# Kernel optimization log

Measured on AMD Instinct MI355X. Metric: run time of the kernel, lower is better.

## Reference

```python
import jax, jax.numpy as jnp
import numpy as np

B, T = 4096, 16384

def setup_inputs() -> dict:
    key = jax.random.key(0)
    ks = jax.random.split(key, 6)
    x = jax.random.normal(ks[0], (B, T), dtype=jnp.float32)
    v0 = jnp.zeros((B, 2), dtype=jnp.float32)
    # match torch init ranges: b* ~ U(-1,1), a* ~ U(-0.5,0.5) (stable region)
    b0 = jax.random.uniform(ks[1], (1,), jnp.float32, -1.0, 1.0)
    b1 = jax.random.uniform(ks[2], (1,), jnp.float32, -1.0, 1.0)
    b2 = jax.random.uniform(ks[3], (1,), jnp.float32, -1.0, 1.0)
    a1 = jax.random.uniform(ks[4], (1,), jnp.float32, -0.5, 0.5)
    a2 = jax.random.uniform(ks[5], (1,), jnp.float32, -0.5, 0.5)
    return {"x": x, "v0": v0, "b0": b0, "b1": b1, "b2": b2, "a1": a1, "a2": a2}

def reference(x, v0, b0, b1, b2, a1, a2):
    """DF-II transposed biquad, scanned over time.
    x: [B, T] input samples; v0: [B, 2] initial state.
    Returns (y [B, T], v_final [B, 2]).
    Per-step math is exactly DTDFIICell.forward:
      y   = x_t * b0 + v[:,0]
      v0' = x_t * b1 + v[:,1] - y * a1
      v1' = x_t * b2            - y * a2
    """
    def step(v, xt):  # v: [B,2], xt: [B]
        y = xt * b0 + v[:, 0]                      # [B]
        v_new = jnp.stack(
            [xt * b1 + v[:, 1] - y * a1,
             xt * b2 - y * a2], axis=-1)           # [B,2]
        return v_new, y
    v_final, ys = jax.lax.scan(step, v0, x.T)      # ys: [T, B]
    return ys.T, v_final
```

## Files before the change

kernel.cpp:

```cpp
#include <hip/hip_runtime.h>

#define B_DIM 4096
#define T_DIM 16384
#define WAVES_PER_BLOCK 4
#define PER_LANE 8
#define CHUNK (64 * PER_LANE)
#define NIT (T_DIM / CHUNK)
#define VSTEP (CHUNK / 4)

typedef float f32x4 __attribute__((ext_vector_type(4)));

struct M2 { float a, b, c, d; };

__device__ inline M2 m2mul(const M2& X, const M2& Y) {
    M2 r;
    r.a = fmaf(X.a, Y.a, X.b * Y.c);
    r.b = fmaf(X.a, Y.b, X.b * Y.d);
    r.c = fmaf(X.c, Y.a, X.d * Y.c);
    r.d = fmaf(X.c, Y.b, X.d * Y.d);
    return r;
}

__global__ __launch_bounds__(256) void biquad_scan_kernel(
    const float* __restrict__ x, const float* __restrict__ v0in,
    const float* __restrict__ pb0, const float* __restrict__ pb1,
    const float* __restrict__ pb2, const float* __restrict__ pa1,
    const float* __restrict__ pa2,
    float* __restrict__ y, float* __restrict__ vout)
{
    const int lane = threadIdx.x & 63;
    const int wave = threadIdx.x >> 6;
    const int row  = blockIdx.x * WAVES_PER_BLOCK + wave;
    if (row >= B_DIM) return;

    const float b0 = *pb0, b1 = *pb1, b2 = *pb2, a1 = *pa1, a2 = *pa2;
    const float na1 = -a1, na2 = -a2;
    const float c0 = b1 - a1 * b0;
    const float c1 = b2 - a2 * b0;

    M2 A  { na1, 1.0f, na2, 0.0f };
    M2 A2 = m2mul(A, A);
    M2 A4 = m2mul(A2, A2);
    M2 A8 = m2mul(A4, A4);

    M2 S0, S1, S2, S3, S4, S5;
    M2 Q { 1.f, 0.f, 0.f, 1.f };
    M2 M = A8;
    S0 = M; if (lane & 1)  Q = m2mul(M, Q); M = m2mul(M, M);
    S1 = M; if (lane & 2)  Q = m2mul(M, Q); M = m2mul(M, M);
    S2 = M; if (lane & 4)  Q = m2mul(M, Q); M = m2mul(M, M);
    S3 = M; if (lane & 8)  Q = m2mul(M, Q); M = m2mul(M, M);
    S4 = M; if (lane & 16) Q = m2mul(M, Q); M = m2mul(M, M);
    S5 = M; if (lane & 32) Q = m2mul(M, Q); M = m2mul(M, M);
    const M2 R = M;

    const float* xr = x + (size_t)row * T_DIM;
    float*       yr = y + (size_t)row * T_DIM;

    float vc0 = v0in[row * 2 + 0];
    float vc1 = v0in[row * 2 + 1];

    const f32x4* xp = (const f32x4*)xr + 2 * lane;
    f32x4*       yp = (f32x4*)yr + 2 * lane;

    f32x4 xa  = xp[0],     xb  = xp[1];
    f32x4 nxa = xp[VSTEP], nxb = xp[VSTEP + 1];

    for (int i = 0; i < NIT; ++i) {
        f32x4 mxa = {0.f, 0.f, 0.f, 0.f}, mxb = {0.f, 0.f, 0.f, 0.f};
        if (i + 2 < NIT) {
            mxa = xp[(size_t)(i + 2) * VSTEP];
            mxb = xp[(size_t)(i + 2) * VSTEP + 1];
        }

        float d0 = c0 * xa[0];
        float d1 = c1 * xa[0];
        #define FOLD(xs)                                               \
        {   float t0 = fmaf(c0, (xs), fmaf(na1, d0, d1));              \
            float t1 = fmaf(na2, d0, c1 * (xs));                       \
            d0 = t0; d1 = t1; }
        FOLD(xa[1]) FOLD(xa[2]) FOLD(xa[3])
        FOLD(xb[0]) FOLD(xb[1]) FOLD(xb[2]) FOLD(xb[3])
        #undef FOLD

        #define SCAN_STEP(Sm, o)                                        \
        {   float q0 = __shfl_up(d0, (unsigned)(o));                    \
            float q1 = __shfl_up(d1, (unsigned)(o));                    \
            if (lane < (o)) { q0 = 0.f; q1 = 0.f; }                     \
            float t0 = fmaf(Sm.a, q0, fmaf(Sm.b, q1, d0));              \
            float t1 = fmaf(Sm.c, q0, fmaf(Sm.d, q1, d1));              \
            d0 = t0; d1 = t1; }
        SCAN_STEP(S0, 1)
        SCAN_STEP(S1, 2)
        SCAN_STEP(S2, 4)
        SCAN_STEP(S3, 8)
        SCAN_STEP(S4, 16)
        SCAN_STEP(S5, 32)
        #undef SCAN_STEP

        float e0 = __shfl_up(d0, 1u);
        float e1 = __shfl_up(d1, 1u);
        if (lane == 0) { e0 = 0.f; e1 = 0.f; }

        float v0r = fmaf(Q.a, vc0, fmaf(Q.b, vc1, e0));
        float v1r = fmaf(Q.c, vc0, fmaf(Q.d, vc1, e1));

        f32x4 yo0, yo1;
        #define REPLAY(xs, dst)                                        \
        {   float yy = fmaf((xs), b0, v0r);                            \
            float n0 = fmaf(na1, yy, fmaf((xs), b1, v1r));             \
            float n1 = fmaf(na2, yy, (xs) * b2);                       \
            v0r = n0; v1r = n1; dst = yy; }
        REPLAY(xa[0], yo0[0]) REPLAY(xa[1], yo0[1])
        REPLAY(xa[2], yo0[2]) REPLAY(xa[3], yo0[3])
        REPLAY(xb[0], yo1[0]) REPLAY(xb[1], yo1[1])
        REPLAY(xb[2], yo1[2]) REPLAY(xb[3], yo1[3])
        #undef REPLAY

        yp[(size_t)i * VSTEP]     = yo0;
        yp[(size_t)i * VSTEP + 1] = yo1;

        float t0 = __shfl(d0, 63);
        float t1 = __shfl(d1, 63);
        float nv0 = fmaf(R.a, vc0, fmaf(R.b, vc1, t0));
        float nv1 = fmaf(R.c, vc0, fmaf(R.d, vc1, t1));
        vc0 = nv0; vc1 = nv1;

        xa = nxa; xb = nxb; nxa = mxa; nxb = mxb;
    }

    if (lane == 0) {
        vout[row * 2 + 0] = vc0;
        vout[row * 2 + 1] = vc1;
    }
}

extern "C" void kernel_launch(void* const* d_in, const int* in_sizes, int n_in,
                              void* d_out, int out_size, void* d_ws, size_t ws_size,
                              hipStream_t stream) {
    const float* x   = (const float*)d_in[0];
    const float* v0  = (const float*)d_in[1];
    const float* b0  = (const float*)d_in[2];
    const float* b1  = (const float*)d_in[3];
    const float* b2  = (const float*)d_in[4];
    const float* a1  = (const float*)d_in[5];
    const float* a2  = (const float*)d_in[6];

    float* y    = (float*)d_out;
    float* vout = (float*)d_out + (size_t)B_DIM * T_DIM;

    dim3 grid(B_DIM / WAVES_PER_BLOCK);
    dim3 block(64 * WAVES_PER_BLOCK);
    biquad_scan_kernel<<<grid, block, 0, stream>>>(x, v0, b0, b1, b2, a1, a2, y, vout);
}
```

Baseline: 118.5 us.

## Split each chunk into two independent 256-sample scans with coalesced float4 access

Each iteration's 512-sample chunk is now two 256-sample halves, with each lane taking 4 contiguous samples per half instead of 8. Lanes therefore read and write consecutive float4s, which makes the global accesses fully coalesced. The two halves are folded, scanned and replayed as independent chains, so their instructions can interleave and hide latency. The cost is twice as many shuffles per chunk and an extra serial state hop between the halves, with the lookback powers recomputed starting from A^4.

After: 118.0 us. No clear change (-0.4%).

```diff
diff --git a/kernel.cpp b/kernel.cpp
--- a/kernel.cpp
+++ b/kernel.cpp
@@ -3,8 +3,7 @@
 #define B_DIM 4096
 #define T_DIM 16384
 #define WAVES_PER_BLOCK 4
-#define PER_LANE 8
-#define CHUNK (64 * PER_LANE)
+#define CHUNK 512
 #define NIT (T_DIM / CHUNK)
 #define VSTEP (CHUNK / 4)
 
@@ -41,11 +40,10 @@
     M2 A  { na1, 1.0f, na2, 0.0f };
     M2 A2 = m2mul(A, A);
     M2 A4 = m2mul(A2, A2);
-    M2 A8 = m2mul(A4, A4);
 
     M2 S0, S1, S2, S3, S4, S5;
     M2 Q { 1.f, 0.f, 0.f, 1.f };
-    M2 M = A8;
+    M2 M = A4;
     S0 = M; if (lane & 1)  Q = m2mul(M, Q); M = m2mul(M, M);
     S1 = M; if (lane & 2)  Q = m2mul(M, Q); M = m2mul(M, M);
     S2 = M; if (lane & 4)  Q = m2mul(M, Q); M = m2mul(M, M);
@@ -60,73 +58,85 @@
     float vc0 = v0in[row * 2 + 0];
     float vc1 = v0in[row * 2 + 1];
 
-    const f32x4* xp = (const f32x4*)xr + 2 * lane;
-    f32x4*       yp = (f32x4*)yr + 2 * lane;
+    const f32x4* xp = (const f32x4*)xr;
+    f32x4*       yp = (f32x4*)yr;
 
-    f32x4 xa  = xp[0],     xb  = xp[1];
-    f32x4 nxa = xp[VSTEP], nxb = xp[VSTEP + 1];
+    f32x4 cA = xp[lane],         cB = xp[64 + lane];
+    f32x4 nA = xp[VSTEP + lane], nB = xp[VSTEP + 64 + lane];
 
     for (int i = 0; i < NIT; ++i) {
-        f32x4 mxa = {0.f, 0.f, 0.f, 0.f}, mxb = {0.f, 0.f, 0.f, 0.f};
+        f32x4 mA = {0.f, 0.f, 0.f, 0.f}, mB = {0.f, 0.f, 0.f, 0.f};
         if (i + 2 < NIT) {
-            mxa = xp[(size_t)(i + 2) * VSTEP];
-            mxb = xp[(size_t)(i + 2) * VSTEP + 1];
+            mA = xp[(size_t)(i + 2) * VSTEP + lane];
+            mB = xp[(size_t)(i + 2) * VSTEP + 64 + lane];
         }
 
-        float d0 = c0 * xa[0];
-        float d1 = c1 * xa[0];
-        #define FOLD(xs)                                               \
-        {   float t0 = fmaf(c0, (xs), fmaf(na1, d0, d1));              \
-            float t1 = fmaf(na2, d0, c1 * (xs));                       \
-            d0 = t0; d1 = t1; }
-        FOLD(xa[1]) FOLD(xa[2]) FOLD(xa[3])
-        FOLD(xb[0]) FOLD(xb[1]) FOLD(xb[2]) FOLD(xb[3])
-        #undef FOLD
+        float dA0 = c0 * cA[0], dA1 = c1 * cA[0];
+        float dB0 = c0 * cB[0], dB1 = c1 * cB[0];
+        #define FOLD2(xsA, xsB)                                          \
+        {   float tA0 = fmaf(c0, (xsA), fmaf(na1, dA0, dA1));            \
+            float tA1 = fmaf(na2, dA0, c1 * (xsA));                      \
+            float tB0 = fmaf(c0, (xsB), fmaf(na1, dB0, dB1));            \
+            float tB1 = fmaf(na2, dB0, c1 * (xsB));                      \
+            dA0 = tA0; dA1 = tA1; dB0 = tB0; dB1 = tB1; }
+        FOLD2(cA[1], cB[1]) FOLD2(cA[2], cB[2]) FOLD2(cA[3], cB[3])
+        #undef FOLD2
 
-        #define SCAN_STEP(Sm, o)                                        \
-        {   float q0 = __shfl_up(d0, (unsigned)(o));                    \
-            float q1 = __shfl_up(d1, (unsigned)(o));                    \
-            if (lane < (o)) { q0 = 0.f; q1 = 0.f; }                     \
-            float t0 = fmaf(Sm.a, q0, fmaf(Sm.b, q1, d0));              \
-            float t1 = fmaf(Sm.c, q0, fmaf(Sm.d, q1, d1));              \
-            d0 = t0; d1 = t1; }
-        SCAN_STEP(S0, 1)
-        SCAN_STEP(S1, 2)
-        SCAN_STEP(S2, 4)
-        SCAN_STEP(S3, 8)
-        SCAN_STEP(S4, 16)
-        SCAN_STEP(S5, 32)
-        #undef SCAN_STEP
+        #define SCAN2(Sm, o)                                             \
+        {   float qA0 = __shfl_up(dA0, (unsigned)(o));                   \
+            float qA1 = __shfl_up(dA1, (unsigned)(o));                   \
+            float qB0 = __shfl_up(dB0, (unsigned)(o));                   \
+            float qB1 = __shfl_up(dB1, (unsigned)(o));                   \
+            if (lane < (o)) { qA0 = 0.f; qA1 = 0.f; qB0 = 0.f; qB1 = 0.f; } \
+            float tA0 = fmaf(Sm.a, qA0, fmaf(Sm.b, qA1, dA0));           \
+            float tA1 = fmaf(Sm.c, qA0, fmaf(Sm.d, qA1, dA1));           \
+            float tB0 = fmaf(Sm.a, qB0, fmaf(Sm.b, qB1, dB0));           \
+            float tB1 = fmaf(Sm.c, qB0, fmaf(Sm.d, qB1, dB1));           \
+            dA0 = tA0; dA1 = tA1; dB0 = tB0; dB1 = tB1; }
+        SCAN2(S0, 1)
+        SCAN2(S1, 2)
+        SCAN2(S2, 4)
+        SCAN2(S3, 8)
+        SCAN2(S4, 16)
+        SCAN2(S5, 32)
+        #undef SCAN2
 
-        float e0 = __shfl_up(d0, 1u);
-        float e1 = __shfl_up(d1, 1u);
-        if (lane == 0) { e0 = 0.f; e1 = 0.f; }
+        float eA0 = __shfl_up(dA0, 1u), eA1 = __shfl_up(dA1, 1u);
+        float eB0 = __shfl_up(dB0, 1u), eB1 = __shfl_up(dB1, 1u);
+        if (lane == 0) { eA0 = 0.f; eA1 = 0.f; eB0 = 0.f; eB1 = 0.f; }
 
-        float v0r = fmaf(Q.a, vc0, fmaf(Q.b, vc1, e0));
-        float v1r = fmaf(Q.c, vc0, fmaf(Q.d, vc1, e1));
+        const float TA0 = __shfl(dA0, 63), TA1 = __shfl(dA1, 63);
+        const float TB0 = __shfl(dB0, 63), TB1 = __shfl(dB1, 63);
 
-        f32x4 yo0, yo1;
-        #define REPLAY(xs, dst)                                        \
-        {   float yy = fmaf((xs), b0, v0r);                            \
-            float n0 = fmaf(na1, yy, fmaf((xs), b1, v1r));             \
-            float n1 = fmaf(na2, yy, (xs) * b2);                       \
-            v0r = n0; v1r = n1; dst = yy; }
-        REPLAY(xa[0], yo0[0]) REPLAY(xa[1], yo0[1])
-        REPLAY(xa[2], yo0[2]) REPLAY(xa[3], yo0[3])
-        REPLAY(xb[0], yo1[0]) REPLAY(xb[1], yo1[1])
-        REPLAY(xb[2], yo1[2]) REPLAY(xb[3], yo1[3])
-        #undef REPLAY
+        float vA0 = fmaf(Q.a, vc0, fmaf(Q.b, vc1, eA0));
+        float vA1 = fmaf(Q.c, vc0, fmaf(Q.d, vc1, eA1));
+        const float sB0 = fmaf(R.a, vc0, fmaf(R.b, vc1, TA0));
+        const float sB1 = fmaf(R.c, vc0, fmaf(R.d, vc1, TA1));
+        float vB0 = fmaf(Q.a, sB0, fmaf(Q.b, sB1, eB0));
+        float vB1 = fmaf(Q.c, sB0, fmaf(Q.d, sB1, eB1));
 
-        yp[(size_t)i * VSTEP]     = yo0;
-        yp[(size_t)i * VSTEP + 1] = yo1;
+        f32x4 yoA, yoB;
+        #define REPLAY2(k)                                               \
+        {   float xsA = cA[k], xsB = cB[k];                              \
+            float yyA = fmaf(xsA, b0, vA0);                              \
+            float yyB = fmaf(xsB, b0, vB0);                              \
+            float nA0 = fmaf(na1, yyA, fmaf(xsA, b1, vA1));              \
+            float nA1 = fmaf(na2, yyA, xsA * b2);                        \
+            float nB0 = fmaf(na1, yyB, fmaf(xsB, b1, vB1));              \
+            float nB1 = fmaf(na2, yyB, xsB * b2);                        \
+            vA0 = nA0; vA1 = nA1; vB0 = nB0; vB1 = nB1;                  \
+            yoA[k] = yyA; yoB[k] = yyB; }
+        REPLAY2(0) REPLAY2(1) REPLAY2(2) REPLAY2(3)
+        #undef REPLAY2
 
-        float t0 = __shfl(d0, 63);
-        float t1 = __shfl(d1, 63);
-        float nv0 = fmaf(R.a, vc0, fmaf(R.b, vc1, t0));
-        float nv1 = fmaf(R.c, vc0, fmaf(R.d, vc1, t1));
+        yp[(size_t)i * VSTEP + lane]      = yoA;
+        yp[(size_t)i * VSTEP + 64 + lane] = yoB;
+
+        const float nv0 = fmaf(R.a, sB0, fmaf(R.b, sB1, TB0));
+        const float nv1 = fmaf(R.c, sB0, fmaf(R.d, sB1, TB1));
         vc0 = nv0; vc1 = nv1;
 
-        xa = nxa; xb = nxb; nxa = mxa; nxb = mxb;
+        cA = nA; cB = nB; nA = mA; nB = mB;
     }
 
     if (lane == 0) {
```

## Use DPP row shifts and broadcasts for the wave scan with 4 samples per lane

Applied to the files above, without the earlier changes.

Shrinks the per-lane chunk from 8 to 4 samples, giving 256-sample chunks and twice as many iterations. The cross-lane linear-recurrence scan switches from ds_bpermute-based __shfl_up to DPP row_shr steps within each row of 16 lanes, then row_bcast15/31 steps with precomputed transition matrices (P, G) to combine rows. The chunk total is read with readlane instead of a shuffle. This cuts shuffle latency on the serial chain per chunk but doubles the number of chunk iterations and uses 16-byte loads and stores per lane instead of 32-byte ones.

After: 114.5 us. 3.4% less time.

```diff
diff --git a/kernel.cpp b/kernel.cpp
--- a/kernel.cpp
+++ b/kernel.cpp
@@ -3,10 +3,8 @@
 #define B_DIM 4096
 #define T_DIM 16384
 #define WAVES_PER_BLOCK 4
-#define PER_LANE 8
-#define CHUNK (64 * PER_LANE)
+#define CHUNK 256
 #define NIT (T_DIM / CHUNK)
-#define VSTEP (CHUNK / 4)
 
 typedef float f32x4 __attribute__((ext_vector_type(4)));
 
@@ -20,6 +18,17 @@
     r.d = fmaf(X.c, Y.b, X.d * Y.d);
     return r;
 }
+
+template<int CTRL, int RMASK>
+__device__ inline float dpp0(float v) {
+    int r = __builtin_amdgcn_update_dpp(0, __builtin_bit_cast(int, v),
+                                        CTRL, RMASK, 0xf, true);
+    return __builtin_bit_cast(float, r);
+}
+
+#define DPP_ROW_SHR(N) (0x110 + (N))
+#define DPP_BCAST15    0x142
+#define DPP_BCAST31    0x143
 
 __global__ __launch_bounds__(256) void biquad_scan_kernel(
     const float* __restrict__ x, const float* __restrict__ v0in,
@@ -41,18 +50,32 @@
     M2 A  { na1, 1.0f, na2, 0.0f };
     M2 A2 = m2mul(A, A);
     M2 A4 = m2mul(A2, A2);
-    M2 A8 = m2mul(A4, A4);
 
     M2 S0, S1, S2, S3, S4, S5;
+    M2 M = A4;
+    S0 = M; M = m2mul(M, M);
+    S1 = M; M = m2mul(M, M);
+    S2 = M; M = m2mul(M, M);
+    S3 = M; M = m2mul(M, M);
+    S4 = M; M = m2mul(M, M);
+    S5 = M; M = m2mul(M, M);
+    const M2 R = M;
+
     M2 Q { 1.f, 0.f, 0.f, 1.f };
-    M2 M = A8;
-    S0 = M; if (lane & 1)  Q = m2mul(M, Q); M = m2mul(M, M);
-    S1 = M; if (lane & 2)  Q = m2mul(M, Q); M = m2mul(M, M);
-    S2 = M; if (lane & 4)  Q = m2mul(M, Q); M = m2mul(M, M);
-    S3 = M; if (lane & 8)  Q = m2mul(M, Q); M = m2mul(M, M);
-    S4 = M; if (lane & 16) Q = m2mul(M, Q); M = m2mul(M, M);
-    S5 = M; if (lane & 32) Q = m2mul(M, Q); M = m2mul(M, M);
-    const M2 R = M;
+    if (lane & 1)  Q = m2mul(S0, Q);
+    if (lane & 2)  Q = m2mul(S1, Q);
+    if (lane & 4)  Q = m2mul(S2, Q);
+    if (lane & 8)  Q = m2mul(S3, Q);
+    if (lane & 16) Q = m2mul(S4, Q);
+    if (lane & 32) Q = m2mul(S5, Q);
+
+    const int l4 = lane & 15;
+    M2 P = A4;
+    if (l4 & 1) P = m2mul(S0, P);
+    if (l4 & 2) P = m2mul(S1, P);
+    if (l4 & 4) P = m2mul(S2, P);
+    if (l4 & 8) P = m2mul(S3, P);
+    M2 G = (lane >= 48) ? m2mul(S4, P) : P;
 
     const float* xr = x + (size_t)row * T_DIM;
     float*       yr = y + (size_t)row * T_DIM;
@@ -60,43 +83,52 @@
     float vc0 = v0in[row * 2 + 0];
     float vc1 = v0in[row * 2 + 1];
 
-    const f32x4* xp = (const f32x4*)xr + 2 * lane;
-    f32x4*       yp = (f32x4*)yr + 2 * lane;
+    const f32x4* xp = (const f32x4*)xr;
+    f32x4*       yp = (f32x4*)yr;
 
-    f32x4 xa  = xp[0],     xb  = xp[1];
-    f32x4 nxa = xp[VSTEP], nxb = xp[VSTEP + 1];
+    f32x4 xv = xp[lane];
+    f32x4 xn = xp[64 + lane];
 
     for (int i = 0; i < NIT; ++i) {
-        f32x4 mxa = {0.f, 0.f, 0.f, 0.f}, mxb = {0.f, 0.f, 0.f, 0.f};
-        if (i + 2 < NIT) {
-            mxa = xp[(size_t)(i + 2) * VSTEP];
-            mxb = xp[(size_t)(i + 2) * VSTEP + 1];
-        }
+        f32x4 xm = {0.f, 0.f, 0.f, 0.f};
+        if (i + 2 < NIT) xm = xp[(size_t)(i + 2) * 64 + lane];
 
-        float d0 = c0 * xa[0];
-        float d1 = c1 * xa[0];
+        float d0 = c0 * xv[0];
+        float d1 = c1 * xv[0];
         #define FOLD(xs)                                               \
         {   float t0 = fmaf(c0, (xs), fmaf(na1, d0, d1));              \
             float t1 = fmaf(na2, d0, c1 * (xs));                       \
             d0 = t0; d1 = t1; }
-        FOLD(xa[1]) FOLD(xa[2]) FOLD(xa[3])
-        FOLD(xb[0]) FOLD(xb[1]) FOLD(xb[2]) FOLD(xb[3])
+        FOLD(xv[1]) FOLD(xv[2]) FOLD(xv[3])
         #undef FOLD
 
-        #define SCAN_STEP(Sm, o)                                        \
-        {   float q0 = __shfl_up(d0, (unsigned)(o));                    \
-            float q1 = __shfl_up(d1, (unsigned)(o));                    \
-            if (lane < (o)) { q0 = 0.f; q1 = 0.f; }                     \
-            float t0 = fmaf(Sm.a, q0, fmaf(Sm.b, q1, d0));              \
-            float t1 = fmaf(Sm.c, q0, fmaf(Sm.d, q1, d1));              \
+        #define SCAN_DPP(Sm, o)                                        \
+        {   float q0 = dpp0<DPP_ROW_SHR(o), 0xf>(d0);                  \
+            float q1 = dpp0<DPP_ROW_SHR(o), 0xf>(d1);                  \
+            float t0 = fmaf(Sm.a, q0, fmaf(Sm.b, q1, d0));             \
+            float t1 = fmaf(Sm.c, q0, fmaf(Sm.d, q1, d1));             \
             d0 = t0; d1 = t1; }
-        SCAN_STEP(S0, 1)
-        SCAN_STEP(S1, 2)
-        SCAN_STEP(S2, 4)
-        SCAN_STEP(S3, 8)
-        SCAN_STEP(S4, 16)
-        SCAN_STEP(S5, 32)
-        #undef SCAN_STEP
+        SCAN_DPP(S0, 1)
+        SCAN_DPP(S1, 2)
+        SCAN_DPP(S2, 4)
+        SCAN_DPP(S3, 8)
+        #undef SCAN_DPP
+
+        {   float q0 = dpp0<DPP_BCAST15, 0xa>(d0);
+            float q1 = dpp0<DPP_BCAST15, 0xa>(d1);
+            float t0 = fmaf(P.a, q0, fmaf(P.b, q1, d0));
+            float t1 = fmaf(P.c, q0, fmaf(P.d, q1, d1));
+            d0 = t0; d1 = t1; }
+        {   float q0 = dpp0<DPP_BCAST31, 0xc>(d0);
+            float q1 = dpp0<DPP_BCAST31, 0xc>(d1);
+            float t0 = fmaf(G.a, q0, fmaf(G.b, q1, d0));
+            float t1 = fmaf(G.c, q0, fmaf(G.d, q1, d1));
+            d0 = t0; d1 = t1; }
+
+        const float T0 = __builtin_bit_cast(float,
+            __builtin_amdgcn_readlane(__builtin_bit_cast(int, d0), 63));
+        const float T1 = __builtin_bit_cast(float,
+            __builtin_amdgcn_readlane(__builtin_bit_cast(int, d1), 63));
 
         float e0 = __shfl_up(d0, 1u);
         float e1 = __shfl_up(d1, 1u);
@@ -105,28 +137,23 @@
         float v0r = fmaf(Q.a, vc0, fmaf(Q.b, vc1, e0));
         float v1r = fmaf(Q.c, vc0, fmaf(Q.d, vc1, e1));
 
-        f32x4 yo0, yo1;
+        f32x4 yv;
         #define REPLAY(xs, dst)                                        \
         {   float yy = fmaf((xs), b0, v0r);                            \
             float n0 = fmaf(na1, yy, fmaf((xs), b1, v1r));             \
             float n1 = fmaf(na2, yy, (xs) * b2);                       \
             v0r = n0; v1r = n1; dst = yy; }
-        REPLAY(xa[0], yo0[0]) REPLAY(xa[1], yo0[1])
-        REPLAY(xa[2], yo0[2]) REPLAY(xa[3], yo0[3])
-        REPLAY(xb[0], yo1[0]) REPLAY(xb[1], yo1[1])
-        REPLAY(xb[2], yo1[2]) REPLAY(xb[3], yo1[3])
+        REPLAY(xv[0], yv[0]) REPLAY(xv[1], yv[1])
+        REPLAY(xv[2], yv[2]) REPLAY(xv[3], yv[3])
         #undef REPLAY
 
-        yp[(size_t)i * VSTEP]     = yo0;
-        yp[(size_t)i * VSTEP + 1] = yo1;
+        yp[(size_t)i * 64 + lane] = yv;
 
-        float t0 = __shfl(d0, 63);
-        float t1 = __shfl(d1, 63);
-        float nv0 = fmaf(R.a, vc0, fmaf(R.b, vc1, t0));
-        float nv1 = fmaf(R.c, vc0, fmaf(R.d, vc1, t1));
+        float nv0 = fmaf(R.a, vc0, fmaf(R.b, vc1, T0));
+        float nv1 = fmaf(R.c, vc0, fmaf(R.d, vc1, T1));
         vc0 = nv0; vc1 = nv1;
 
-        xa = nxa; xb = nxb; nxa = mxa; nxb = mxb;
+        xv = xn; xn = xm;
     }
 
     if (lane == 0) {
```

## Split each row across four waves with cross-wave carry via shared memory

Applied to the files above, without the earlier changes.

Each block now handles one row instead of four. The four waves each process consecutive 256-sample chunks of a 1024-sample super-chunk, with 4 samples per lane instead of 8. Wave carries are exchanged through double-buffered shared memory with a __syncthreads per super-chunk, and each wave composes the preceding waves' carries using the chunk transition matrix. This shortens each wave's serial fold and replay chain and increases row-level parallelism, but it adds a block barrier and LDS traffic every iteration, plus redundant carry composition.

After: 111.3 us. 1.06x faster.

```diff
diff --git a/kernel.cpp b/kernel.cpp
--- a/kernel.cpp
+++ b/kernel.cpp
@@ -2,11 +2,9 @@
 
 #define B_DIM 4096
 #define T_DIM 16384
-#define WAVES_PER_BLOCK 4
-#define PER_LANE 8
-#define CHUNK (64 * PER_LANE)
-#define NIT (T_DIM / CHUNK)
-#define VSTEP (CHUNK / 4)
+#define NWAVES 4
+#define CHUNK 256
+#define NSUP (T_DIM / (CHUNK * NWAVES))
 
 typedef float f32x4 __attribute__((ext_vector_type(4)));
 
@@ -29,9 +27,8 @@
     float* __restrict__ y, float* __restrict__ vout)
 {
     const int lane = threadIdx.x & 63;
-    const int wave = threadIdx.x >> 6;
-    const int row  = blockIdx.x * WAVES_PER_BLOCK + wave;
-    if (row >= B_DIM) return;
+    const int w    = threadIdx.x >> 6;
+    const int row  = blockIdx.x;
 
     const float b0 = *pb0, b1 = *pb1, b2 = *pb2, a1 = *pa1, a2 = *pa2;
     const float na1 = -a1, na2 = -a2;
@@ -41,11 +38,10 @@
     M2 A  { na1, 1.0f, na2, 0.0f };
     M2 A2 = m2mul(A, A);
     M2 A4 = m2mul(A2, A2);
-    M2 A8 = m2mul(A4, A4);
 
     M2 S0, S1, S2, S3, S4, S5;
     M2 Q { 1.f, 0.f, 0.f, 1.f };
-    M2 M = A8;
+    M2 M = A4;
     S0 = M; if (lane & 1)  Q = m2mul(M, Q); M = m2mul(M, M);
     S1 = M; if (lane & 2)  Q = m2mul(M, Q); M = m2mul(M, M);
     S2 = M; if (lane & 4)  Q = m2mul(M, Q); M = m2mul(M, M);
@@ -54,33 +50,29 @@
     S5 = M; if (lane & 32) Q = m2mul(M, Q); M = m2mul(M, M);
     const M2 R = M;
 
-    const float* xr = x + (size_t)row * T_DIM;
-    float*       yr = y + (size_t)row * T_DIM;
+    __shared__ float Tb[2][NWAVES][2];
+
+    const f32x4* xp = (const f32x4*)(x + (size_t)row * T_DIM);
+    f32x4*       yp = (f32x4*)(y + (size_t)row * T_DIM);
 
     float vc0 = v0in[row * 2 + 0];
     float vc1 = v0in[row * 2 + 1];
 
-    const f32x4* xp = (const f32x4*)xr + 2 * lane;
-    f32x4*       yp = (f32x4*)yr + 2 * lane;
+    f32x4 xv = xp[(size_t)(0 * NWAVES + w) * 64 + lane];
+    f32x4 xn = xp[(size_t)(1 * NWAVES + w) * 64 + lane];
 
-    f32x4 xa  = xp[0],     xb  = xp[1];
-    f32x4 nxa = xp[VSTEP], nxb = xp[VSTEP + 1];
+    for (int s = 0; s < NSUP; ++s) {
+        f32x4 xm = {0.f, 0.f, 0.f, 0.f};
+        if (s + 2 < NSUP)
+            xm = xp[(size_t)((s + 2) * NWAVES + w) * 64 + lane];
 
-    for (int i = 0; i < NIT; ++i) {
-        f32x4 mxa = {0.f, 0.f, 0.f, 0.f}, mxb = {0.f, 0.f, 0.f, 0.f};
-        if (i + 2 < NIT) {
-            mxa = xp[(size_t)(i + 2) * VSTEP];
-            mxb = xp[(size_t)(i + 2) * VSTEP + 1];
-        }
-
-        float d0 = c0 * xa[0];
-        float d1 = c1 * xa[0];
+        float d0 = c0 * xv[0];
+        float d1 = c1 * xv[0];
         #define FOLD(xs)                                               \
         {   float t0 = fmaf(c0, (xs), fmaf(na1, d0, d1));              \
             float t1 = fmaf(na2, d0, c1 * (xs));                       \
             d0 = t0; d1 = t1; }
-        FOLD(xa[1]) FOLD(xa[2]) FOLD(xa[3])
-        FOLD(xb[0]) FOLD(xb[1]) FOLD(xb[2]) FOLD(xb[3])
+        FOLD(xv[1]) FOLD(xv[2]) FOLD(xv[3])
         #undef FOLD
 
         #define SCAN_STEP(Sm, o)                                        \
@@ -101,35 +93,58 @@
         float e0 = __shfl_up(d0, 1u);
         float e1 = __shfl_up(d1, 1u);
         if (lane == 0) { e0 = 0.f; e1 = 0.f; }
+        const float T0 = __shfl(d0, 63);
+        const float T1 = __shfl(d1, 63);
 
-        float v0r = fmaf(Q.a, vc0, fmaf(Q.b, vc1, e0));
-        float v1r = fmaf(Q.c, vc0, fmaf(Q.d, vc1, e1));
+        if (lane == 0) { Tb[s & 1][w][0] = T0; Tb[s & 1][w][1] = T1; }
+        __syncthreads();
 
-        f32x4 yo0, yo1;
+        const float t00 = Tb[s & 1][0][0], t01 = Tb[s & 1][0][1];
+        const float t10 = Tb[s & 1][1][0], t11 = Tb[s & 1][1][1];
+        const float t20 = Tb[s & 1][2][0], t21 = Tb[s & 1][2][1];
+        const float t30 = Tb[s & 1][3][0], t31 = Tb[s & 1][3][1];
+
+        float s0 = vc0, s1 = vc1;
+        #define APPLY(u0, u1)                                          \
+        {   float n0 = fmaf(R.a, s0, fmaf(R.b, s1, (u0)));             \
+            float n1 = fmaf(R.c, s0, fmaf(R.d, s1, (u1)));             \
+            s0 = n0; s1 = n1; }
+        if (w > 0) APPLY(t00, t01)
+        if (w > 1) APPLY(t10, t11)
+        if (w > 2) APPLY(t20, t21)
+        #undef APPLY
+
+        {
+            float u0 = vc0, u1 = vc1;
+            #define APPLYU(q0, q1)                                     \
+            {   float n0 = fmaf(R.a, u0, fmaf(R.b, u1, (q0)));         \
+                float n1 = fmaf(R.c, u0, fmaf(R.d, u1, (q1)));         \
+                u0 = n0; u1 = n1; }
+            APPLYU(t00, t01) APPLYU(t10, t11)
+            APPLYU(t20, t21) APPLYU(t30, t31)
+            #undef APPLYU
+            vc0 = u0; vc1 = u1;
+        }
+
+        float v0r = fmaf(Q.a, s0, fmaf(Q.b, s1, e0));
+        float v1r = fmaf(Q.c, s0, fmaf(Q.d, s1, e1));
+
+        f32x4 yv;
         #define REPLAY(xs, dst)                                        \
         {   float yy = fmaf((xs), b0, v0r);                            \
             float n0 = fmaf(na1, yy, fmaf((xs), b1, v1r));             \
             float n1 = fmaf(na2, yy, (xs) * b2);                       \
             v0r = n0; v1r = n1; dst = yy; }
-        REPLAY(xa[0], yo0[0]) REPLAY(xa[1], yo0[1])
-        REPLAY(xa[2], yo0[2]) REPLAY(xa[3], yo0[3])
-        REPLAY(xb[0], yo1[0]) REPLAY(xb[1], yo1[1])
-        REPLAY(xb[2], yo1[2]) REPLAY(xb[3], yo1[3])
+        REPLAY(xv[0], yv[0]) REPLAY(xv[1], yv[1])
+        REPLAY(xv[2], yv[2]) REPLAY(xv[3], yv[3])
         #undef REPLAY
 
-        yp[(size_t)i * VSTEP]     = yo0;
-        yp[(size_t)i * VSTEP + 1] = yo1;
+        yp[(size_t)(s * NWAVES + w) * 64 + lane] = yv;
 
-        float t0 = __shfl(d0, 63);
-        float t1 = __shfl(d1, 63);
-        float nv0 = fmaf(R.a, vc0, fmaf(R.b, vc1, t0));
-        float nv1 = fmaf(R.c, vc0, fmaf(R.d, vc1, t1));
-        vc0 = nv0; vc1 = nv1;
-
-        xa = nxa; xb = nxb; nxa = mxa; nxb = mxb;
+        xv = xn; xn = xm;
     }
 
-    if (lane == 0) {
+    if (threadIdx.x == 0) {
         vout[row * 2 + 0] = vc0;
         vout[row * 2 + 1] = vc1;
     }
@@ -149,7 +164,7 @@
     float* y    = (float*)d_out;
     float* vout = (float*)d_out + (size_t)B_DIM * T_DIM;
 
-    dim3 grid(B_DIM / WAVES_PER_BLOCK);
-    dim3 block(64 * WAVES_PER_BLOCK);
+    dim3 grid(B_DIM);
+    dim3 block(64 * NWAVES);
     biquad_scan_kernel<<<grid, block, 0, stream>>>(x, v0, b0, b1, b2, a1, a2, y, vout);
 }
```
